# Kernel optimization log

Hardware: AMD Instinct MI355X
Metric: run time of the kernel (lower is better)

Reference implementation:

```python
import jax, jax.numpy as jnp
import numpy as np

NUM_ITERATIONS = 3
B, M, P, D, O, I = 32, 32, 196, 20, 16, 8


def squash(s, axis=-1):
    # v = (||s||^2 / (1+||s||^2)) * s/||s||
    sq = jnp.sum(s * s, axis=axis, keepdims=True)
    return (sq / (1.0 + sq)) * s / jnp.sqrt(sq + 1e-9)


def setup_inputs() -> dict:
    key = jax.random.key(0)
    kx, kw = jax.random.split(key)
    x = jax.random.normal(kx, (B, M, P, I), dtype=jnp.float32)
    W = jax.random.normal(kw, (1, M, P, D, O, I), dtype=jnp.float32)
    return {"x": x, "W": W}


def reference(x, W):
    b_, m, p, i = x.shape
    Wm = W[0]  # [M,P,D,O,I]
    # u_hat = W @ u : batched matvec -> [B,M,P,D,O]
    u_hat = jnp.einsum('mpdoi,bmpi->bmpdo', Wm, x)
    d = u_hat.shape[3]
    b = jnp.zeros((b_, m, p, d), dtype=x.dtype)
    c = None
    v = None
    for it in range(NUM_ITERATIONS):
        # softmax jointly over (num_in_caps * num_digit_cap), matching view+softmax(dim=2)
        c = jax.nn.softmax(b.reshape(b_, m, p * d), axis=2).reshape(b_, m, p, d)
        # s = sum over maps and in-caps of c * u_hat -> [B,D,O]
        s = jnp.einsum('bmpd,bmpdo->bdo', c, u_hat)
        v = squash(s, axis=-1)
        if it != NUM_ITERATIONS - 1:
            # agreement: u_hat^T v -> [B,M,P,D]
            b = b + jnp.einsum('bmpdo,bdo->bmpd', u_hat, v)
    map_size = int(np.sqrt(p))
    weighted = c[..., None] * u_hat  # [B,M,P,D,O]
    xm = weighted.reshape(b_, m, map_size, map_size, d, -1)
    c_maps = jnp.sqrt(jnp.sum(xm * xm, axis=-1))  # [B,M,ms,ms,D]
    features = jnp.mean(weighted, axis=2)  # [B,M,D,O]
    return v, c_maps, features
```

## Files before the change

kernel.cpp:

```cpp
#include <hip/hip_runtime.h>
#include <math.h>

#define B_   32
#define M_   32
#define P_   196
#define D_   20
#define O_   16
#define I_   8
#define DO_  320
#define PD_  3920
#define ROW_ 62720

#define CMAPS_OFF 10240
#define FEAT_OFF  4024320

__device__ __forceinline__ unsigned short f2bf(float v) {
    unsigned int u = __float_as_uint(v);
    return (unsigned short)((u + 0x7fffu + ((u >> 16) & 1u)) >> 16);
}
__device__ __forceinline__ unsigned int pk2(float lo, float hi) {
    return (unsigned int)f2bf(lo) | ((unsigned int)f2bf(hi) << 16);
}
__device__ __forceinline__ float bfhi(unsigned int w) { return __uint_as_float(w & 0xffff0000u); }
__device__ __forceinline__ float bflo(unsigned int w) { return __uint_as_float(w << 16); }

__device__ __forceinline__ void gload16(const float* g, float* l) {
    __builtin_amdgcn_global_load_lds(
        (const __attribute__((address_space(1))) void*)g,
        (__attribute__((address_space(3))) void*)l, 16, 0, 0);
}

#define CPT_ 4
#define CNT_ 49
__global__ __launch_bounds__(320)
void caps_u(const float* __restrict__ x, const float* __restrict__ W,
            unsigned short* __restrict__ uh)
{
    __shared__ float4 wb[2][1280];
    __shared__ float  xl[1024];

    const int m  = blockIdx.x / CNT_;
    const int pt = blockIdx.x % CNT_;
    const int p0 = pt * CPT_;
    const int t  = threadIdx.x;
    const int g  = t % 40;
    const int bq = t / 40;
    const int wl = t & ~63;

    if (t < 256) {
        int b = t >> 3, q = t & 7;
        *(float4*)(xl + b * 32 + q * 4) =
            *(const float4*)(x + (((size_t)b * M_ + m) * P_ + p0) * I_ + q * 4);
    }
    {
        const float* ws0 = W + (size_t)(m * P_ + p0) * 2560;
        #pragma unroll
        for (int q = 0; q < 4; q++) {
            int s = q * 320 + t;
            gload16(ws0 + (size_t)(s ^ ((s >> 4) & 7)) * 4,
                    (float*)&wb[0][q * 320 + wl]);
        }
    }
    __syncthreads();

    #pragma unroll
    for (int h = 0; h < 2; h++) {
        if (h == 0) {
            const float* ws1 = W + (size_t)(m * P_ + p0 + 2) * 2560;
            #pragma unroll
            for (int q = 0; q < 4; q++) {
                int s = q * 320 + t;
                gload16(ws1 + (size_t)(s ^ ((s >> 4) & 7)) * 4,
                        (float*)&wb[1][q * 320 + wl]);
            }
        }
        #pragma unroll
        for (int pp = 0; pp < 2; pp++) {
            const int pl = 2 * h + pp;
            float xr[4][8];
            #pragma unroll
            for (int bb = 0; bb < 4; bb++) {
                *(float4*)(xr[bb])     = *(float4*)(xl + (bq * 4 + bb) * 32 + pl * 8);
                *(float4*)(xr[bb] + 4) = *(float4*)(xl + (bq * 4 + bb) * 32 + pl * 8 + 4);
            }
            const float4* wp = &wb[h][pp * 640];
            #pragma unroll
            for (int r = 0; r < 4; r++) {
                const int gb = 4 * g + 160 * r;
                const int hx = (gb >> 4) & 7;
                float4 w0 = wp[(gb + 0) ^ hx];
                float4 w1 = wp[(gb + 1) ^ hx];
                float4 w2 = wp[(gb + 2) ^ hx];
                float4 w3 = wp[(gb + 3) ^ hx];
                const int do0 = 2 * g + 80 * r;
                #pragma unroll
                for (int bb = 0; bb < 4; bb++) {
                    const float* a = xr[bb];
                    float u0 = w0.x * a[0];
                    u0 = fmaf(w0.y, a[1], u0); u0 = fmaf(w0.z, a[2], u0);
                    u0 = fmaf(w0.w, a[3], u0); u0 = fmaf(w1.x, a[4], u0);
                    u0 = fmaf(w1.y, a[5], u0); u0 = fmaf(w1.z, a[6], u0);
                    u0 = fmaf(w1.w, a[7], u0);
                    float u1 = w2.x * a[0];
                    u1 = fmaf(w2.y, a[1], u1); u1 = fmaf(w2.z, a[2], u1);
                    u1 = fmaf(w2.w, a[3], u1); u1 = fmaf(w3.x, a[4], u1);
                    u1 = fmaf(w3.y, a[5], u1); u1 = fmaf(w3.z, a[6], u1);
                    u1 = fmaf(w3.w, a[7], u1);
                    *(unsigned int*)(uh + (((size_t)(bq * 4 + bb) * M_ + m) * P_
                                           + p0 + pl) * DO_ + do0) = pk2(u0, u1);
                }
            }
        }
        if (h == 0) __syncthreads();
    }
}

template<int MODE>
__global__ __launch_bounds__(320)
void route_k(const unsigned short* __restrict__ uh, const float* __restrict__ vin,
             float* __restrict__ pbm, float* __restrict__ out)
{
    extern __shared__ float sm[];
    float* accL  = sm;
    float* red   = sm + 320 * 17;
    float* blogL = red + 16;
    float* usqL  = blogL + 3920;

    const int blk = blockIdx.x;
    const int t = threadIdx.x;
    const int d = t % 20;
    const int k = t / 20;
    const int pstart = k * 12 + (k < 4 ? k : 4);
    const int pcnt   = (k < 4) ? 13 : 12;
    const unsigned short* up = uh + (size_t)blk * ROW_ + d * 16;

    float vreg[16];
    if (MODE) {
        const float* vb = vin + (size_t)(blk >> 5) * DO_;
        #pragma unroll
        for (int o = 0; o < 16; o++) vreg[o] = vb[d * 16 + o];
    }
    float acc[16];
    #pragma unroll
    for (int o = 0; o < 16; o++) acc[o] = 0.f;
    float mloc = -1e30f, Z = 0.f;

    float4 a0 = ((const float4*)(up + (size_t)pstart * DO_))[0];
    float4 a1 = ((const float4*)(up + (size_t)pstart * DO_))[1];

    for (int pp = 0; pp < pcnt; pp++) {
        const int p  = pstart + pp;
        const int pn = pstart + ((pp + 1 < pcnt) ? pp + 1 : pp);
        float4 n0 = ((const float4*)(up + (size_t)pn * DO_))[0];
        float4 n1 = ((const float4*)(up + (size_t)pn * DO_))[1];

        unsigned int ua[8];
        ua[0]=__float_as_uint(a0.x); ua[1]=__float_as_uint(a0.y);
        ua[2]=__float_as_uint(a0.z); ua[3]=__float_as_uint(a0.w);
        ua[4]=__float_as_uint(a1.x); ua[5]=__float_as_uint(a1.y);
        ua[6]=__float_as_uint(a1.z); ua[7]=__float_as_uint(a1.w);
        float u[16];
        #pragma unroll
        for (int q = 0; q < 8; q++) { u[2*q] = bflo(ua[q]); u[2*q+1] = bfhi(ua[q]); }

        if (MODE) {
            float bl = u[0] * vreg[0];
            #pragma unroll
            for (int o = 1; o < 16; o++) bl = fmaf(u[o], vreg[o], bl);
            if (MODE == 2) {
                float us = u[0] * u[0];
                #pragma unroll
                for (int o = 1; o < 16; o++) us = fmaf(u[o], u[o], us);
                blogL[p * D_ + d] = bl;
                usqL[p * D_ + d]  = us;
            }
            if (bl > mloc + 8.f) {
                float r = __expf(mloc - bl);
                Z *= r;
                #pragma unroll
                for (int o = 0; o < 16; o++) acc[o] *= r;
                mloc = bl;
            }
            float e = __expf(bl - mloc);
            Z += e;
            #pragma unroll
            for (int o = 0; o < 16; o++) acc[o] = fmaf(e, u[o], acc[o]);
        } else {
            #pragma unroll
            for (int o = 0; o < 16; o++) acc[o] += u[o];
        }
        a0 = n0; a1 = n1;
    }

    float f = 1.f, iz = 1.f, mx = 0.f;
    if (MODE) {
        mx = mloc;
        #pragma unroll
        for (int msk = 1; msk < 64; msk <<= 1) mx = fmaxf(mx, __shfl_xor(mx, msk, 64));
        if ((t & 63) == 0) red[t >> 6] = mx;
        __syncthreads();
        mx = fmaxf(fmaxf(fmaxf(red[0], red[1]), fmaxf(red[2], red[3])), red[4]);
        f = __expf(mloc - mx);
        float zz = Z * f;
        #pragma unroll
        for (int msk = 1; msk < 64; msk <<= 1) zz += __shfl_xor(zz, msk, 64);
        if ((t & 63) == 0) red[8 + (t >> 6)] = zz;
        __syncthreads();
        iz = 1.f / (red[8] + red[9] + red[10] + red[11] + red[12]);
    }
    #pragma unroll
    for (int o = 0; o < 16; o++) accL[t * 17 + o] = acc[o] * f;
    __syncthreads();
    {
        const int dd = t >> 4, oo = t & 15;
        float s = 0.f;
        #pragma unroll
        for (int kk = 0; kk < 16; kk++) s += accL[(kk * 20 + dd) * 17 + oo];
        s *= iz;
        pbm[(size_t)blk * DO_ + t] = s;
        if (MODE == 2) out[FEAT_OFF + (size_t)blk * DO_ + t] = s * (1.f / 196.f);
    }
    if (MODE == 2) {
        for (int e = t; e < PD_; e += 320)
            out[CMAPS_OFF + (size_t)blk * PD_ + e] =
                __expf(blogL[e] - mx) * iz * sqrtf(usqL[e]);
    }
}

template<int WH>
__global__ __launch_bounds__(320)
void sq2_k(const float* __restrict__ pbm, float* __restrict__ v1,
           float* __restrict__ vs, float* __restrict__ out)
{
    const int b = blockIdx.x, t = threadIdx.x;
    float s = 0.f;
    for (int mi = 0; mi < M_; mi++) s += pbm[((size_t)b * M_ + mi) * DO_ + t];
    if (WH == 0) s *= (1.f / PD_);
    float sq = s * s;
    #pragma unroll
    for (int msk = 1; msk < 16; msk <<= 1) sq += __shfl_xor(sq, msk, 16);
    float vr = (sq / (1.f + sq)) * s * rsqrtf(sq + 1e-9f);
    if (WH == 0) v1[(size_t)b * DO_ + t] = vr;
    if (WH == 1) vs[(size_t)b * DO_ + t] = v1[(size_t)b * DO_ + t] + vr;
    if (WH == 2) out[(size_t)b * DO_ + t] = vr;
}

extern "C" void kernel_launch(void* const* d_in, const int* in_sizes, int n_in,
                              void* d_out, int out_size, void* d_ws, size_t ws_size,
                              hipStream_t stream)
{
    const float* x = (const float*)d_in[0];
    const float* W = (const float*)d_in[1];
    float* out = (float*)d_out;

    unsigned short* uh = (unsigned short*)d_ws;
    float* fws = (float*)((char*)d_ws + (size_t)64225280 * 2);
    float* pbm = fws;
    float* v1  = pbm + (size_t)B_ * M_ * DO_;
    float* vs  = v1 + (size_t)B_ * DO_;

    const size_t LDS_A = (320 * 17 + 16) * sizeof(float);
    const size_t LDS_B = LDS_A + 2 * PD_ * sizeof(float);

    caps_u<<<M_ * CNT_, 320, 0, stream>>>(x, W, uh);

    route_k<0><<<B_ * M_, 320, LDS_A, stream>>>(uh, v1, pbm, out);
    sq2_k<0><<<B_, 320, 0, stream>>>(pbm, v1, vs, out);

    route_k<1><<<B_ * M_, 320, LDS_A, stream>>>(uh, v1, pbm, out);
    sq2_k<1><<<B_, 320, 0, stream>>>(pbm, v1, vs, out);

    route_k<2><<<B_ * M_, 320, LDS_B, stream>>>(uh, vs, pbm, out);
    sq2_k<2><<<B_, 320, 0, stream>>>(pbm, v1, vs, out);
}
```

Measured before the change: 122.5 us.

## Fuse first routing iteration into u_hat kernel via atomic partial sums

The first routing pass, which uses uniform coupling and so is just a sum of u_hat, is folded into the u_hat producer kernel. Each block accumulates per-thread partial sums and atomically adds them into four replicated buffers that a small kernel then reduces. This removes one full pass reading the bf16 u_hat tensor. It also halves the positions per block to double the grid, adds a memset, and unrolls the routing loop by two. In exchange it adds many float atomics and makes the summation order nondeterministic.

```diff
diff --git a/kernel.cpp b/kernel.cpp
--- a/kernel.cpp
+++ b/kernel.cpp
@@ -30,14 +30,14 @@
         (__attribute__((address_space(3))) void*)l, 16, 0, 0);
 }
 
-#define CPT_ 4
-#define CNT_ 49
+#define CPT_ 2
+#define CNT_ 98
 __global__ __launch_bounds__(320)
 void caps_u(const float* __restrict__ x, const float* __restrict__ W,
-            unsigned short* __restrict__ uh)
+            unsigned short* __restrict__ uh, float* __restrict__ s1r)
 {
-    __shared__ float4 wb[2][1280];
-    __shared__ float  xl[1024];
+    __shared__ float4 wb[2][640];
+    __shared__ float  xl[512];
 
     const int m  = blockIdx.x / CNT_;
     const int pt = blockIdx.x % CNT_;
@@ -47,15 +47,16 @@
     const int bq = t / 40;
     const int wl = t & ~63;
 
-    if (t < 256) {
-        int b = t >> 3, q = t & 7;
-        *(float4*)(xl + b * 32 + q * 4) =
-            *(const float4*)(x + (((size_t)b * M_ + m) * P_ + p0) * I_ + q * 4);
+    if (t < 128) {
+        int b = t >> 2, q = t & 3;
+        *(float4*)(xl + b * 16 + q * 4) =
+            *(const float4*)(x + (((size_t)b * M_ + m) * P_ + p0 + (q >> 1)) * I_
+                             + (q & 1) * 4);
     }
     {
         const float* ws0 = W + (size_t)(m * P_ + p0) * 2560;
         #pragma unroll
-        for (int q = 0; q < 4; q++) {
+        for (int q = 0; q < 2; q++) {
             int s = q * 320 + t;
             gload16(ws0 + (size_t)(s ^ ((s >> 4) & 7)) * 4,
                     (float*)&wb[0][q * 320 + wl]);
@@ -63,55 +64,70 @@
     }
     __syncthreads();
 
+    float acc_s[4][4][2];
+    #pragma unroll
+    for (int bb = 0; bb < 4; bb++)
+        #pragma unroll
+        for (int r = 0; r < 4; r++) { acc_s[bb][r][0] = 0.f; acc_s[bb][r][1] = 0.f; }
+
     #pragma unroll
     for (int h = 0; h < 2; h++) {
         if (h == 0) {
-            const float* ws1 = W + (size_t)(m * P_ + p0 + 2) * 2560;
+            const float* ws1 = W + (size_t)(m * P_ + p0 + 1) * 2560;
             #pragma unroll
-            for (int q = 0; q < 4; q++) {
+            for (int q = 0; q < 2; q++) {
                 int s = q * 320 + t;
                 gload16(ws1 + (size_t)(s ^ ((s >> 4) & 7)) * 4,
                         (float*)&wb[1][q * 320 + wl]);
             }
         }
-        #pragma unroll
-        for (int pp = 0; pp < 2; pp++) {
-            const int pl = 2 * h + pp;
-            float xr[4][8];
+        const int pl = h;
+        float xr[4][8];
+        #pragma unroll
+        for (int bb = 0; bb < 4; bb++) {
+            *(float4*)(xr[bb])     = *(float4*)(xl + (bq * 4 + bb) * 16 + pl * 8);
+            *(float4*)(xr[bb] + 4) = *(float4*)(xl + (bq * 4 + bb) * 16 + pl * 8 + 4);
+        }
+        const float4* wp = wb[h];
+        #pragma unroll
+        for (int r = 0; r < 4; r++) {
+            const int gb = 4 * g + 160 * r;
+            const int hx = (gb >> 4) & 7;
+            float4 w0 = wp[(gb + 0) ^ hx];
+            float4 w1 = wp[(gb + 1) ^ hx];
+            float4 w2 = wp[(gb + 2) ^ hx];
+            float4 w3 = wp[(gb + 3) ^ hx];
+            const int do0 = 2 * g + 80 * r;
             #pragma unroll
             for (int bb = 0; bb < 4; bb++) {
-                *(float4*)(xr[bb])     = *(float4*)(xl + (bq * 4 + bb) * 32 + pl * 8);
-                *(float4*)(xr[bb] + 4) = *(float4*)(xl + (bq * 4 + bb) * 32 + pl * 8 + 4);
+                const float* a = xr[bb];
+                float u0 = w0.x * a[0];
+                u0 = fmaf(w0.y, a[1], u0); u0 = fmaf(w0.z, a[2], u0);
+                u0 = fmaf(w0.w, a[3], u0); u0 = fmaf(w1.x, a[4], u0);
+                u0 = fmaf(w1.y, a[5], u0); u0 = fmaf(w1.z, a[6], u0);
+                u0 = fmaf(w1.w, a[7], u0);
+                float u1 = w2.x * a[0];
+                u1 = fmaf(w2.y, a[1], u1); u1 = fmaf(w2.z, a[2], u1);
+                u1 = fmaf(w2.w, a[3], u1); u1 = fmaf(w3.x, a[4], u1);
+                u1 = fmaf(w3.y, a[5], u1); u1 = fmaf(w3.z, a[6], u1);
+                u1 = fmaf(w3.w, a[7], u1);
+                acc_s[bb][r][0] += u0; acc_s[bb][r][1] += u1;
+                *(unsigned int*)(uh + (((size_t)(bq * 4 + bb) * M_ + m) * P_
+                                       + p0 + pl) * DO_ + do0) = pk2(u0, u1);
             }
-            const float4* wp = &wb[h][pp * 640];
-            #pragma unroll
-            for (int r = 0; r < 4; r++) {
-                const int gb = 4 * g + 160 * r;
-                const int hx = (gb >> 4) & 7;
-                float4 w0 = wp[(gb + 0) ^ hx];
-                float4 w1 = wp[(gb + 1) ^ hx];
-                float4 w2 = wp[(gb + 2) ^ hx];
-                float4 w3 = wp[(gb + 3) ^ hx];
-                const int do0 = 2 * g + 80 * r;
-                #pragma unroll
-                for (int bb = 0; bb < 4; bb++) {
-                    const float* a = xr[bb];
-                    float u0 = w0.x * a[0];
-                    u0 = fmaf(w0.y, a[1], u0); u0 = fmaf(w0.z, a[2], u0);
-                    u0 = fmaf(w0.w, a[3], u0); u0 = fmaf(w1.x, a[4], u0);
-                    u0 = fmaf(w1.y, a[5], u0); u0 = fmaf(w1.z, a[6], u0);
-                    u0 = fmaf(w1.w, a[7], u0);
-                    float u1 = w2.x * a[0];
-                    u1 = fmaf(w2.y, a[1], u1); u1 = fmaf(w2.z, a[2], u1);
-                    u1 = fmaf(w2.w, a[3], u1); u1 = fmaf(w3.x, a[4], u1);
-                    u1 = fmaf(w3.y, a[5], u1); u1 = fmaf(w3.z, a[6], u1);
-                    u1 = fmaf(w3.w, a[7], u1);
-                    *(unsigned int*)(uh + (((size_t)(bq * 4 + bb) * M_ + m) * P_
-                                           + p0 + pl) * DO_ + do0) = pk2(u0, u1);
-                }
-            }
         }
         if (h == 0) __syncthreads();
+    }
+    float* s1p = s1r + (blockIdx.x & 3) * (B_ * DO_);
+    #pragma unroll
+    for (int bb = 0; bb < 4; bb++) {
+        const int b = bq * 4 + bb;
+        #pragma unroll
+        for (int r = 0; r < 4; r++) {
+            const int do0 = 2 * g + 80 * r;
+            atomicAdd(s1p + b * DO_ + do0,     acc_s[bb][r][0]);
+            atomicAdd(s1p + b * DO_ + do0 + 1, acc_s[bb][r][1]);
+        }
     }
 }
 
@@ -135,7 +151,7 @@
     const unsigned short* up = uh + (size_t)blk * ROW_ + d * 16;
 
     float vreg[16];
-    if (MODE) {
+    {
         const float* vb = vin + (size_t)(blk >> 5) * DO_;
         #pragma unroll
         for (int o = 0; o < 16; o++) vreg[o] = vb[d * 16 + o];
@@ -145,55 +161,65 @@
     for (int o = 0; o < 16; o++) acc[o] = 0.f;
     float mloc = -1e30f, Z = 0.f;
 
-    float4 a0 = ((const float4*)(up + (size_t)pstart * DO_))[0];
-    float4 a1 = ((const float4*)(up + (size_t)pstart * DO_))[1];
-
-    for (int pp = 0; pp < pcnt; pp++) {
-        const int p  = pstart + pp;
-        const int pn = pstart + ((pp + 1 < pcnt) ? pp + 1 : pp);
-        float4 n0 = ((const float4*)(up + (size_t)pn * DO_))[0];
-        float4 n1 = ((const float4*)(up + (size_t)pn * DO_))[1];
-
-        unsigned int ua[8];
-        ua[0]=__float_as_uint(a0.x); ua[1]=__float_as_uint(a0.y);
-        ua[2]=__float_as_uint(a0.z); ua[3]=__float_as_uint(a0.w);
-        ua[4]=__float_as_uint(a1.x); ua[5]=__float_as_uint(a1.y);
-        ua[6]=__float_as_uint(a1.z); ua[7]=__float_as_uint(a1.w);
-        float u[16];
-        #pragma unroll
-        for (int q = 0; q < 8; q++) { u[2*q] = bflo(ua[q]); u[2*q+1] = bfhi(ua[q]); }
-
-        if (MODE) {
-            float bl = u[0] * vreg[0];
-            #pragma unroll
-            for (int o = 1; o < 16; o++) bl = fmaf(u[o], vreg[o], bl);
-            if (MODE == 2) {
-                float us = u[0] * u[0];
-                #pragma unroll
-                for (int o = 1; o < 16; o++) us = fmaf(u[o], u[o], us);
-                blogL[p * D_ + d] = bl;
-                usqL[p * D_ + d]  = us;
-            }
-            if (bl > mloc + 8.f) {
-                float r = __expf(mloc - bl);
-                Z *= r;
-                #pragma unroll
-                for (int o = 0; o < 16; o++) acc[o] *= r;
-                mloc = bl;
-            }
-            float e = __expf(bl - mloc);
-            Z += e;
-            #pragma unroll
-            for (int o = 0; o < 16; o++) acc[o] = fmaf(e, u[o], acc[o]);
-        } else {
-            #pragma unroll
-            for (int o = 0; o < 16; o++) acc[o] += u[o];
-        }
-        a0 = n0; a1 = n1;
-    }
-
-    float f = 1.f, iz = 1.f, mx = 0.f;
-    if (MODE) {
+    float4 c0a, c0b, c1a, c1b;
+    c0a = ((const float4*)(up + (size_t)pstart * DO_))[0];
+    c0b = ((const float4*)(up + (size_t)pstart * DO_))[1];
+    {
+        int p1 = pstart + (pcnt > 1 ? 1 : 0);
+        c1a = ((const float4*)(up + (size_t)p1 * DO_))[0];
+        c1b = ((const float4*)(up + (size_t)p1 * DO_))[1];
+    }
+
+#define PROC(A0, A1, PIDX)                                                    \
+    {                                                                         \
+        unsigned int ua[8];                                                   \
+        ua[0]=__float_as_uint(A0.x); ua[1]=__float_as_uint(A0.y);             \
+        ua[2]=__float_as_uint(A0.z); ua[3]=__float_as_uint(A0.w);             \
+        ua[4]=__float_as_uint(A1.x); ua[5]=__float_as_uint(A1.y);             \
+        ua[6]=__float_as_uint(A1.z); ua[7]=__float_as_uint(A1.w);             \
+        float u[16];                                                          \
+        _Pragma("unroll")                                                     \
+        for (int q = 0; q < 8; q++) { u[2*q] = bflo(ua[q]); u[2*q+1] = bfhi(ua[q]); } \
+        float bl = u[0] * vreg[0];                                            \
+        _Pragma("unroll")                                                     \
+        for (int o = 1; o < 16; o++) bl = fmaf(u[o], vreg[o], bl);            \
+        if (MODE == 2) {                                                      \
+            float us = u[0] * u[0];                                           \
+            _Pragma("unroll")                                                 \
+            for (int o = 1; o < 16; o++) us = fmaf(u[o], u[o], us);           \
+            blogL[(PIDX) * D_ + d] = bl;                                      \
+            usqL[(PIDX) * D_ + d]  = us;                                      \
+        }                                                                     \
+        if (bl > mloc + 8.f) {                                                \
+            float rr = __expf(mloc - bl);                                     \
+            Z *= rr;                                                          \
+            _Pragma("unroll")                                                 \
+            for (int o = 0; o < 16; o++) acc[o] *= rr;                        \
+            mloc = bl;                                                        \
+        }                                                                     \
+        float e = __expf(bl - mloc);                                          \
+        Z += e;                                                               \
+        _Pragma("unroll")                                                     \
+        for (int o = 0; o < 16; o++) acc[o] = fmaf(e, u[o], acc[o]);          \
+    }
+
+    int pp = 0;
+    for (; pp + 1 < pcnt; pp += 2) {
+        int pn0 = pstart + ((pp + 2 < pcnt) ? pp + 2 : pcnt - 1);
+        int pn1 = pstart + ((pp + 3 < pcnt) ? pp + 3 : pcnt - 1);
+        float4 n0a = ((const float4*)(up + (size_t)pn0 * DO_))[0];
+        float4 n0b = ((const float4*)(up + (size_t)pn0 * DO_))[1];
+        float4 n1a = ((const float4*)(up + (size_t)pn1 * DO_))[0];
+        float4 n1b = ((const float4*)(up + (size_t)pn1 * DO_))[1];
+        PROC(c0a, c0b, pstart + pp);
+        PROC(c1a, c1b, pstart + pp + 1);
+        c0a = n0a; c0b = n0b; c1a = n1a; c1b = n1b;
+    }
+    if (pp < pcnt) PROC(c0a, c0b, pstart + pp);
+#undef PROC
+
+    float f, iz, mx;
+    {
         mx = mloc;
         #pragma unroll
         for (int msk = 1; msk < 64; msk <<= 1) mx = fmaxf(mx, __shfl_xor(mx, msk, 64));
@@ -229,13 +255,19 @@
 
 template<int WH>
 __global__ __launch_bounds__(320)
-void sq2_k(const float* __restrict__ pbm, float* __restrict__ v1,
+void sq2_k(const float* __restrict__ src, float* __restrict__ v1,
            float* __restrict__ vs, float* __restrict__ out)
 {
     const int b = blockIdx.x, t = threadIdx.x;
     float s = 0.f;
-    for (int mi = 0; mi < M_; mi++) s += pbm[((size_t)b * M_ + mi) * DO_ + t];
-    if (WH == 0) s *= (1.f / PD_);
+    if (WH == 0) {
+        #pragma unroll
+        for (int rep = 0; rep < 4; rep++)
+            s += src[rep * (B_ * DO_) + b * DO_ + t];
+        s *= (1.f / PD_);
+    } else {
+        for (int mi = 0; mi < M_; mi++) s += src[((size_t)b * M_ + mi) * DO_ + t];
+    }
     float sq = s * s;
     #pragma unroll
     for (int msk = 1; msk < 16; msk <<= 1) sq += __shfl_xor(sq, msk, 16);
@@ -258,14 +290,15 @@
     float* pbm = fws;
     float* v1  = pbm + (size_t)B_ * M_ * DO_;
     float* vs  = v1 + (size_t)B_ * DO_;
+    float* s1r = vs + (size_t)B_ * DO_;
 
     const size_t LDS_A = (320 * 17 + 16) * sizeof(float);
     const size_t LDS_B = LDS_A + 2 * PD_ * sizeof(float);
 
-    caps_u<<<M_ * CNT_, 320, 0, stream>>>(x, W, uh);
-
-    route_k<0><<<B_ * M_, 320, LDS_A, stream>>>(uh, v1, pbm, out);
-    sq2_k<0><<<B_, 320, 0, stream>>>(pbm, v1, vs, out);
+    hipMemsetAsync(s1r, 0, 4 * (size_t)B_ * DO_ * sizeof(float), stream);
+
+    caps_u<<<M_ * CNT_, 320, 0, stream>>>(x, W, uh, s1r);
+    sq2_k<0><<<B_, 320, 0, stream>>>(s1r, v1, vs, out);
 
     route_k<1><<<B_ * M_, 320, LDS_A, stream>>>(uh, v1, pbm, out);
     sq2_k<1><<<B_, 320, 0, stream>>>(pbm, v1, vs, out);
```

New measurement: 280.2 us. 129% more time.
